# Kernel optimization log

Hardware: AMD Instinct MI355X
Metric: run time of the kernel (lower is better)

## Reference

```python
import jax, jax.numpy as jnp
import numpy as np

N_NODES = 50000
N_EDGES = 600000
N_DISCRETE = 70
NH = N_DISCRETE - 6          # 64
EMB = 128                    # n_embedding
D = NH + EMB                 # 192, resdnn/cross input dim
RES_HID = 512                # l_hidden entries
N_RES = 2                    # len(l_hidden)
N_CROSS = 2
PRED_HID = (2 * NH + 512) // 2  # 320
NEG_SLOPE = 0.01


def setup_inputs() -> dict:
    key = jax.random.key(0)
    ks = jax.random.split(key, 24)
    def w(k, shape, fan_in):
        return (jax.random.normal(k, shape, jnp.float32) / np.sqrt(fan_in)).astype(jnp.float32)
    inp = {
        "discrete_x": jax.random.randint(ks[0], (N_NODES, N_DISCRETE), 0, 100, jnp.int64),
        "edge_index": jax.random.randint(ks[1], (2, N_EDGES), 0, N_NODES, jnp.int64),
        # graph embedding linear + 2 GCN layers
        "w_g0": w(ks[2], (NH, EMB), NH), "b_g0": jnp.zeros((EMB,), jnp.float32),
        "w_gcn1": w(ks[3], (EMB, EMB), EMB), "b_gcn1": jnp.zeros((EMB,), jnp.float32),
        "w_gcn2": w(ks[4], (EMB, EMB), EMB), "b_gcn2": jnp.zeros((EMB,), jnp.float32),
        # ResDNN: N_RES dim-preserving residual bottleneck blocks D->RES_HID->D
        "res_w1": w(ks[5], (N_RES, D, RES_HID), D), "res_b1": jnp.zeros((N_RES, RES_HID), jnp.float32),
        "res_w2": w(ks[6], (N_RES, RES_HID, D), RES_HID), "res_b2": jnp.zeros((N_RES, D), jnp.float32),
        # CrossNet: N_CROSS layers
        "cross_w": w(ks[7], (N_CROSS, D), D), "cross_b": jnp.zeros((N_CROSS, D), jnp.float32),
        # Prediction MLP: 2D -> PRED_HID -> 1, sigmoid
        "p_w1": w(ks[8], (2 * D, PRED_HID), 2 * D), "p_b1": jnp.zeros((PRED_HID,), jnp.float32),
        "p_w2": w(ks[9], (PRED_HID, 1), PRED_HID), "p_b2": jnp.zeros((1,), jnp.float32),
    }
    return inp


def _leaky(x):
    return jax.nn.leaky_relu(x, NEG_SLOPE)


def _gcn_conv(x, W, b, row, col, n):
    # PyG GCNConv: linear, then sym-normalized aggregation over A + I, then bias
    h = x @ W
    deg = jax.ops.segment_sum(jnp.ones(row.shape, x.dtype), col, num_segments=n) + 1.0
    dinv = jax.lax.rsqrt(deg)
    norm = dinv[row] * dinv[col]            # [E]
    msg = h[row] * norm[:, None]            # [E, EMB]  (largest intermediate)
    agg = jax.ops.segment_sum(msg, col, num_segments=n)
    agg = agg + h * (dinv * dinv)[:, None]  # self-loop contribution
    return agg + b


def reference(discrete_x, edge_index, w_g0, b_g0, w_gcn1, b_gcn1, w_gcn2, b_gcn2,
              res_w1, res_b1, res_w2, res_b2, cross_w, cross_b,
              p_w1, p_b1, p_w2, p_b2):
    n = discrete_x.shape[0]
    row, col = edge_index[0], edge_index[1]
    # DiscreteFeatureEmbeddingLayer: map n_discrete_features int cols -> nh float dims
    x_d = discrete_x[:, :NH].astype(jnp.float32)
    # graph branch
    x_g = _leaky(x_d @ w_g0 + b_g0)
    x_g = _leaky(_gcn_conv(x_g, w_gcn1, b_gcn1, row, col, n))
    x_g = _leaky(_gcn_conv(x_g, w_gcn2, b_gcn2, row, col, n))
    x = jnp.concatenate([x_d, x_g], axis=-1)  # [N, D]
    # ResDNN: residual bottleneck blocks
    x_deep = x
    for i in range(N_RES):
        h = _leaky(x_deep @ res_w1[i] + res_b1[i])
        x_deep = _leaky(x_deep + h @ res_w2[i] + res_b2[i])
    # CrossNet (DCN): x_{l+1} = x0 * (x_l . w_l) + b_l + x_l
    x0 = x
    x_cross = x
    for i in range(N_CROSS):
        xw = x_cross @ cross_w[i]            # [N]
        x_cross = x0 * xw[:, None] + cross_b[i] + x_cross
    z = jnp.concatenate([x_deep, x_cross], axis=-1)  # [N, 2D]
    h = _leaky(z @ p_w1 + p_b1)
    y = jax.nn.sigmoid(h @ p_w2 + p_b2)
    return y.squeeze(-1)
```

## Files before the change

kernel.cpp:

```cpp
#include <hip/hip_runtime.h>
#include <math.h>

constexpr int NCOLS   = 70;
constexpr int NH      = 64;
constexpr int EMB     = 128;
constexpr int DD      = 192;
constexpr int RES_HID = 512;
constexpr int PRED_HID= 320;

typedef _Float16 f16x8 __attribute__((ext_vector_type(8)));
typedef float    f32x4 __attribute__((ext_vector_type(4)));
#define MFMA16F(a,b,c) __builtin_amdgcn_mfma_f32_16x16x32_f16((a),(b),(c),0,0,0)

constexpr float LO_SCALE   = 4096.0f;
constexpr float LO_DESCALE = 1.0f/4096.0f;
constexpr float Z_SCALE    = 0.0625f;
constexpr float Z_DESCALE  = 16.0f;

__device__ __forceinline__ float leaky(float x){ return x > 0.f ? x : 0.01f*x; }

__global__ void k_zero(int* p, int n){
  int i = blockIdx.x*256 + threadIdx.x;
  if (i < n) p[i] = 0;
}
__global__ void k_hist(const int* __restrict__ col, int* __restrict__ cnt, int E){
  int e = blockIdx.x*256 + threadIdx.x;
  if (e < E) atomicAdd(&cnt[col[e]], 1);
}
__global__ void k_scanA(const int* __restrict__ cnt, int* __restrict__ bsum, int n){
  __shared__ int s;
  if (threadIdx.x == 0) s = 0;
  __syncthreads();
  int i = blockIdx.x*256 + threadIdx.x;
  int v = (i < n) ? cnt[i] : 0;
  #pragma unroll
  for (int o=32;o;o>>=1) v += __shfl_xor(v, o, 64);
  if ((threadIdx.x & 63) == 0) atomicAdd(&s, v);
  __syncthreads();
  if (threadIdx.x == 0) bsum[blockIdx.x] = s;
}
__global__ void k_scanB(int* bsum, int nb){
  __shared__ int s[256];
  __shared__ int carry;
  if (threadIdx.x == 0) carry = 0;
  __syncthreads();
  for (int start = 0; start < nb; start += 256){
    int i = start + threadIdx.x;
    int v = (i < nb) ? bsum[i] : 0;
    s[threadIdx.x] = v; __syncthreads();
    for (int o=1;o<256;o<<=1){
      int t = (threadIdx.x >= o) ? s[threadIdx.x-o] : 0;
      __syncthreads();
      s[threadIdx.x] += t; __syncthreads();
    }
    if (i < nb) bsum[i] = carry + s[threadIdx.x] - v;
    __syncthreads();
    if (threadIdx.x == 255) carry += s[255];
    __syncthreads();
  }
}
__global__ void k_scanC(const int* __restrict__ cnt, const int* __restrict__ bsum,
                        int* __restrict__ base, int* __restrict__ cursor,
                        float* __restrict__ dinv, int n, int E){
  __shared__ int s[256];
  int i = blockIdx.x*256 + threadIdx.x;
  int v = (i < n) ? cnt[i] : 0;
  s[threadIdx.x] = v; __syncthreads();
  for (int o=1;o<256;o<<=1){
    int t = (threadIdx.x >= o) ? s[threadIdx.x-o] : 0;
    __syncthreads();
    s[threadIdx.x] += t; __syncthreads();
  }
  if (i < n){
    int b = bsum[blockIdx.x] + s[threadIdx.x] - v;
    base[i] = b; cursor[i] = b;
    dinv[i] = rsqrtf((float)(v + 1));
  }
  if (i == n-1) base[n] = E;
}
__global__ void k_fill(const int* __restrict__ row, const int* __restrict__ col,
                       const float* __restrict__ dinv, int* __restrict__ cursor,
                       int2* __restrict__ ebin, int E){
  int e = blockIdx.x*256 + threadIdx.x;
  if (e < E){
    int r = row[e], c = col[e];
    int slot = atomicAdd(&cursor[c], 1);
    ebin[slot] = make_int2(r, __float_as_int(dinv[r]));
  }
}

__global__ void k_wprep_pack(const float* __restrict__ W, _Float16* __restrict__ Wh,
                             _Float16* __restrict__ Wl, int K, int N){
  int idx = blockIdx.x*256 + threadIdx.x;
  if (idx < K*N){
    int k = idx / N, nn = idx - k*N;
    float v = W[idx];
    _Float16 h = (_Float16)v;
    float lo = (v - (float)h)*LO_SCALE;
    int kc = k >> 5, r = k & 31;
    int lane = (nn & 15) | ((r >> 3) << 4);
    int j = r & 7;
    size_t dst = ((size_t)((nn >> 4)*(K >> 5) + kc) << 9) + lane*8 + j;
    Wh[dst] = h;
    Wl[dst] = (_Float16)lo;
  }
}

__global__ void k_embed(const int* __restrict__ dx, float* __restrict__ A, int n){
  int idx = blockIdx.x*256 + threadIdx.x;
  if (idx < n*NH){
    int i = idx >> 6, j = idx & 63;
    A[(size_t)i*DD + j] = (float)dx[(size_t)i*NCOLS + j];
  }
}

template<int K>
__global__ void k_lin(const float* __restrict__ X, int ldx, int xoff,
                      const float* __restrict__ W, const float* __restrict__ bias,
                      float* __restrict__ out, int ldo, int ooff, int n, int act)
{
  constexpr int ST = 20;
  __shared__ __align__(16) float sxT[K*ST];
  int i0 = blockIdx.x*16;
  for (int idx = threadIdx.x; idx < 16*K; idx += 256){
    int t = idx / K, k = idx - t*K;
    int i = i0 + t;
    sxT[k*ST + t] = (i < n) ? X[(size_t)i*ldx + xoff + k] : 0.f;
  }
  __syncthreads();
  int jj = threadIdx.x & 127;
  int tg = threadIdx.x >> 7;
  float b = bias ? bias[jj] : 0.f;
  float acc[8];
  #pragma unroll
  for (int t=0;t<8;t++) acc[t] = b;
  for (int k=0;k<K;k++){
    float w = W[(size_t)k*128 + jj];
    float4 xa = *(const float4*)&sxT[k*ST + tg*8];
    float4 xb = *(const float4*)&sxT[k*ST + tg*8 + 4];
    acc[0] = fmaf(xa.x, w, acc[0]); acc[1] = fmaf(xa.y, w, acc[1]);
    acc[2] = fmaf(xa.z, w, acc[2]); acc[3] = fmaf(xa.w, w, acc[3]);
    acc[4] = fmaf(xb.x, w, acc[4]); acc[5] = fmaf(xb.y, w, acc[5]);
    acc[6] = fmaf(xb.z, w, acc[6]); acc[7] = fmaf(xb.w, w, acc[7]);
  }
  #pragma unroll
  for (int tt=0;tt<8;tt++){
    int i = i0 + tg*8 + tt;
    if (i < n){
      float v = acc[tt];
      if (act) v = leaky(v);
      out[(size_t)i*ldo + ooff + jj] = v;
    }
  }
}

__global__ void k_gather(const float* __restrict__ h, const float* __restrict__ dinv,
                         const int* __restrict__ base, const int2* __restrict__ ebin,
                         const float* __restrict__ bias, float* __restrict__ out,
                         int ldo, int ooff, int n)
{
  int node = blockIdx.x*4 + (threadIdx.x >> 6);
  int lane = threadIdx.x & 63;
  if (node >= n) return;
  int b0 = base[node], b1 = base[node+1];
  float dc = dinv[node];
  float ax = 0.f, ay = 0.f;
  int e = b0;
  for (; e + 1 < b1; e += 2){
    int2 ea = ebin[e], eb = ebin[e+1];
    float2 ha = ((const float2*)(h + (size_t)ea.x*EMB))[lane];
    float2 hb = ((const float2*)(h + (size_t)eb.x*EMB))[lane];
    float da = __int_as_float(ea.y), db = __int_as_float(eb.y);
    ax = fmaf(ha.x, da, ax); ay = fmaf(ha.y, da, ay);
    ax = fmaf(hb.x, db, ax); ay = fmaf(hb.y, db, ay);
  }
  if (e < b1){
    int2 ea = ebin[e];
    float2 ha = ((const float2*)(h + (size_t)ea.x*EMB))[lane];
    float da = __int_as_float(ea.y);
    ax = fmaf(ha.x, da, ax); ay = fmaf(ha.y, da, ay);
  }
  float2 hc = ((const float2*)(h + (size_t)node*EMB))[lane];
  float vx = leaky((ax + hc.x*dc)*dc + bias[2*lane]);
  float vy = leaky((ay + hc.y*dc)*dc + bias[2*lane+1]);
  float* op = out + (size_t)node*ldo + ooff + 2*lane;
  op[0] = vx; op[1] = vy;
}

constexpr int XS = 196;
constexpr int HS = 516;

__global__ __launch_bounds__(256,2)
void k_resblock_mfma(const float* __restrict__ X,
                     const _Float16* __restrict__ W1h, const _Float16* __restrict__ W1l,
                     const float* __restrict__ b1,
                     const _Float16* __restrict__ W2h, const _Float16* __restrict__ W2l,
                     const float* __restrict__ b2,
                     float* __restrict__ out, int n)
{
  __shared__ __align__(16) _Float16 xh[32*XS];
  __shared__ __align__(16) _Float16 xl[32*XS];
  __shared__ __align__(16) _Float16 hh[32*HS];
  int i0 = blockIdx.x*32;
  for (int idx = threadIdx.x; idx < 32*DD; idx += 256){
    int t = idx / DD, k = idx - t*DD;
    int i = i0 + t;
    float v = (i < n) ? X[(size_t)i*DD + k] : 0.f;
    _Float16 h = (_Float16)v;
    xh[t*XS + k] = h;
    xl[t*XS + k] = (_Float16)((v - (float)h)*LO_SCALE);
  }
  __syncthreads();
  int wv = threadIdx.x >> 6, ln = threadIdx.x & 63;
  int cn = ln & 15, kg = ln >> 4;

  {
    f16x8 A0h[6], A0l[6], A1h[6], A1l[6];
    #pragma unroll
    for (int kc=0;kc<6;kc++){
      int k0 = kc*32 + kg*8;
      A0h[kc] = *(const f16x8*)&xh[cn*XS + k0];
      A0l[kc] = *(const f16x8*)&xl[cn*XS + k0];
      A1h[kc] = *(const f16x8*)&xh[(16+cn)*XS + k0];
      A1l[kc] = *(const f16x8*)&xl[(16+cn)*XS + k0];
    }
    float bias1[8];
    #pragma unroll
    for (int ct=0;ct<8;ct++) bias1[ct] = b1[(wv*8+ct)*16 + cn];
    const _Float16* pbh = W1h + ((size_t)(wv*8)*6 << 9) + ln*8;
    const _Float16* pbl = W1l + ((size_t)(wv*8)*6 << 9) + ln*8;
    f16x8 Bh[6], Bl[6];
    #pragma unroll
    for (int kc=0;kc<6;kc++){
      Bh[kc] = *(const f16x8*)(pbh + ((size_t)kc<<9));
      Bl[kc] = *(const f16x8*)(pbl + ((size_t)kc<<9));
    }
    #pragma unroll 1
    for (int ct = 0; ct < 8; ct++){
      f16x8 Bh2[6], Bl2[6];
      if (ct < 7){
        const _Float16* nh = pbh + ((size_t)((ct+1)*6) << 9);
        const _Float16* nl = pbl + ((size_t)((ct+1)*6) << 9);
        #pragma unroll
        for (int kc=0;kc<6;kc++){
          Bh2[kc] = *(const f16x8*)(nh + ((size_t)kc<<9));
          Bl2[kc] = *(const f16x8*)(nl + ((size_t)kc<<9));
        }
      }
      f32x4 acc0={0.f,0.f,0.f,0.f}, accL0={0.f,0.f,0.f,0.f};
      f32x4 acc1={0.f,0.f,0.f,0.f}, accL1={0.f,0.f,0.f,0.f};
      #pragma unroll
      for (int kc=0;kc<6;kc++){
        acc0  = MFMA16F(A0h[kc], Bh[kc], acc0);
        accL0 = MFMA16F(A0l[kc], Bh[kc], accL0);
        accL0 = MFMA16F(A0h[kc], Bl[kc], accL0);
        acc1  = MFMA16F(A1h[kc], Bh[kc], acc1);
        accL1 = MFMA16F(A1l[kc], Bh[kc], accL1);
        accL1 = MFMA16F(A1h[kc], Bl[kc], accL1);
      }
      int n0 = (wv*8+ct)*16;
      float bb = bias1[ct];
      #pragma unroll
      for (int r=0;r<4;r++){
        hh[(kg*4+r)*HS + n0 + cn]    = (_Float16)leaky(acc0[r] + accL0[r]*LO_DESCALE + bb);
        hh[(16+kg*4+r)*HS + n0 + cn] = (_Float16)leaky(acc1[r] + accL1[r]*LO_DESCALE + bb);
      }
      #pragma unroll
      for (int kc=0;kc<6;kc++){ Bh[kc]=Bh2[kc]; Bl[kc]=Bl2[kc]; }
    }
  }
  __syncthreads();

  {
    f32x4 acc[3][2], accL[3][2];
    #pragma unroll
    for (int c=0;c<3;c++){
      #pragma unroll
      for (int g=0;g<2;g++){
        acc[c][g]  = (f32x4){0.f,0.f,0.f,0.f};
        accL[c][g] = (f32x4){0.f,0.f,0.f,0.f};
      }
    }
    f16x8 B2h[3], B2l[3];
    #pragma unroll
    for (int c=0;c<3;c++){
      size_t off = ((size_t)((wv*3+c)*16) << 9) + ln*8;
      B2h[c] = *(const f16x8*)(W2h + off);
      B2l[c] = *(const f16x8*)(W2l + off);
    }
    #pragma unroll 1
    for (int kc=0;kc<16;kc++){
      f16x8 N2h[3], N2l[3];
      if (kc < 15){
        #pragma unroll
        for (int c=0;c<3;c++){
          size_t off = ((size_t)((wv*3+c)*16 + kc + 1) << 9) + ln*8;
          N2h[c] = *(const f16x8*)(W2h + off);
          N2l[c] = *(const f16x8*)(W2l + off);
        }
      }
      int k0 = kc*32 + kg*8;
      f16x8 a0 = *(const f16x8*)&hh[cn*HS + k0];
      f16x8 a1 = *(const f16x8*)&hh[(16+cn)*HS + k0];
      #pragma unroll
      for (int c=0;c<3;c++){
        acc[c][0]  = MFMA16F(a0, B2h[c], acc[c][0]);
        accL[c][0] = MFMA16F(a0, B2l[c], accL[c][0]);
        acc[c][1]  = MFMA16F(a1, B2h[c], acc[c][1]);
        accL[c][1] = MFMA16F(a1, B2l[c], accL[c][1]);
      }
      #pragma unroll
      for (int c=0;c<3;c++){ B2h[c]=N2h[c]; B2l[c]=N2l[c]; }
    }
    #pragma unroll
    for (int c=0;c<3;c++){
      int n0 = (wv*3+c)*16;
      float bb = b2[n0 + cn];
      #pragma unroll
      for (int r=0;r<4;r++){
        int m0 = kg*4 + r, m1 = 16 + kg*4 + r;
        float res0 = (float)xh[m0*XS + n0 + cn] + (float)xl[m0*XS + n0 + cn]*LO_DESCALE;
        float res1 = (float)xh[m1*XS + n0 + cn] + (float)xl[m1*XS + n0 + cn]*LO_DESCALE;
        int ia = i0 + m0, ib = i0 + m1;
        if (ia < n) out[(size_t)ia*DD + n0 + cn] = leaky(res0 + acc[c][0][r] + accL[c][0][r]*LO_DESCALE + bb);
        if (ib < n) out[(size_t)ib*DD + n0 + cn] = leaky(res1 + acc[c][1][r] + accL[c][1][r]*LO_DESCALE + bb);
      }
    }
  }
}

__global__ void k_cross(const float* __restrict__ X0, const float* __restrict__ cw,
                        const float* __restrict__ cb, float* __restrict__ out, int n)
{
  int node = blockIdx.x*4 + (threadIdx.x >> 6);
  int lane = threadIdx.x & 63;
  if (node >= n) return;
  const float* xr = X0 + (size_t)node*DD;
  float v0[3], xc[3];
  #pragma unroll
  for (int m=0;m<3;m++){ v0[m] = xr[lane + 64*m]; xc[m] = v0[m]; }
  #pragma unroll
  for (int l=0;l<2;l++){
    float p = 0.f;
    #pragma unroll
    for (int m=0;m<3;m++) p += xc[m]*cw[l*DD + lane + 64*m];
    #pragma unroll
    for (int off=32; off>0; off>>=1) p += __shfl_xor(p, off, 64);
    #pragma unroll
    for (int m=0;m<3;m++) xc[m] = v0[m]*p + cb[l*DD + lane + 64*m] + xc[m];
  }
  #pragma unroll
  for (int m=0;m<3;m++) out[(size_t)node*DD + lane + 64*m] = xc[m];
}

constexpr int ZS = 392;

__global__ __launch_bounds__(256,3)
void k_pred_mfma(const float* __restrict__ deep, const float* __restrict__ cross,
                 const _Float16* __restrict__ Wh, const _Float16* __restrict__ Wl,
                 const float* __restrict__ b1,
                 const float* __restrict__ w2, const float* __restrict__ b2,
                 float* __restrict__ y, int n)
{
  __shared__ __align__(16) _Float16 zh[32*ZS];
  __shared__ __align__(16) _Float16 zl[32*ZS];
  __shared__ float sred[4][32];
  int i0 = blockIdx.x*32;
  for (int idx = threadIdx.x; idx < 32*2*DD; idx += 256){
    int t = idx / (2*DD), k = idx - t*(2*DD);
    int i = i0 + t;
    float v = 0.f;
    if (i < n) v = (k < DD) ? deep[(size_t)i*DD + k] : cross[(size_t)i*DD + (k - DD)];
    v *= Z_SCALE;
    _Float16 h = (_Float16)v;
    float lo = (v - (float)h)*LO_SCALE;
    zh[t*ZS + k] = h;
    zl[t*ZS + k] = (_Float16)lo;
  }
  __syncthreads();
  int wv = threadIdx.x >> 6, ln = threadIdx.x & 63;
  int cn = ln & 15, kg = ln >> 4;
  float vs0[4] = {0.f,0.f,0.f,0.f};
  float vs1[4] = {0.f,0.f,0.f,0.f};
  #pragma unroll 1
  for (int ct = 0; ct < 5; ct++){
    int nt = wv*5 + ct;
    int n0 = nt*16;
    f32x4 acc0 = {0.f,0.f,0.f,0.f}, accL0 = {0.f,0.f,0.f,0.f};
    f32x4 acc1 = {0.f,0.f,0.f,0.f}, accL1 = {0.f,0.f,0.f,0.f};
    const _Float16* wbh = Wh + ((size_t)nt*12 << 9) + ln*8;
    const _Float16* wbl = Wl + ((size_t)nt*12 << 9) + ln*8;
    #pragma unroll 4
    for (int kc = 0; kc < 12; kc++){
      f16x8 bh = *(const f16x8*)(wbh + (kc << 9));
      f16x8 bl = *(const f16x8*)(wbl + (kc << 9));
      int k0 = kc*32 + kg*8;
      f16x8 a0h = *(const f16x8*)&zh[cn*ZS + k0];
      f16x8 a0l = *(const f16x8*)&zl[cn*ZS + k0];
      f16x8 a1h = *(const f16x8*)&zh[(16+cn)*ZS + k0];
      f16x8 a1l = *(const f16x8*)&zl[(16+cn)*ZS + k0];
      acc0  = MFMA16F(a0h, bh, acc0);
      accL0 = MFMA16F(a0l, bh, accL0);
      accL0 = MFMA16F(a0h, bl, accL0);
      acc1  = MFMA16F(a1h, bh, acc1);
      accL1 = MFMA16F(a1l, bh, accL1);
      accL1 = MFMA16F(a1h, bl, accL1);
    }
    float bb = b1[n0 + cn];
    float ww = w2[n0 + cn];
    #pragma unroll
    for (int r=0;r<4;r++){
      float v0 = (acc0[r] + accL0[r]*LO_DESCALE)*Z_DESCALE + bb;
      float v1 = (acc1[r] + accL1[r]*LO_DESCALE)*Z_DESCALE + bb;
      vs0[r] += leaky(v0)*ww;
      vs1[r] += leaky(v1)*ww;
    }
  }
  #pragma unroll
  for (int r=0;r<4;r++){
    #pragma unroll
    for (int off=1; off<16; off<<=1){
      vs0[r] += __shfl_xor(vs0[r], off, 64);
      vs1[r] += __shfl_xor(vs1[r], off, 64);
    }
  }
  if (cn == 0){
    #pragma unroll
    for (int r=0;r<4;r++){
      sred[wv][kg*4 + r]      = vs0[r];
      sred[wv][16 + kg*4 + r] = vs1[r];
    }
  }
  __syncthreads();
  if (threadIdx.x < 32){
    int m = threadIdx.x;
    float s = sred[0][m] + sred[1][m] + sred[2][m] + sred[3][m] + b2[0];
    int i = i0 + m;
    if (i < n) y[i] = 1.f/(1.f + expf(-s));
  }
}

extern "C" void kernel_launch(void* const* d_in, const int* in_sizes, int n_in,
                              void* d_out, int out_size, void* d_ws, size_t ws_size,
                              hipStream_t stream)
{
  const int*   dx      = (const int*)d_in[0];
  const int*   ei      = (const int*)d_in[1];
  const float* w_g0    = (const float*)d_in[2];
  const float* b_g0    = (const float*)d_in[3];
  const float* w_gcn1  = (const float*)d_in[4];
  const float* b_gcn1  = (const float*)d_in[5];
  const float* w_gcn2  = (const float*)d_in[6];
  const float* b_gcn2  = (const float*)d_in[7];
  const float* res_w1  = (const float*)d_in[8];
  const float* res_b1  = (const float*)d_in[9];
  const float* res_w2  = (const float*)d_in[10];
  const float* res_b2  = (const float*)d_in[11];
  const float* cross_w = (const float*)d_in[12];
  const float* cross_b = (const float*)d_in[13];
  const float* p_w1    = (const float*)d_in[14];
  const float* p_b1    = (const float*)d_in[15];
  const float* p_w2    = (const float*)d_in[16];
  const float* p_b2    = (const float*)d_in[17];
  float* y = (float*)d_out;

  int n = in_sizes[0] / NCOLS;
  int E = in_sizes[1] / 2;
  const int* row = ei;
  const int* col = ei + E;

  float* ws  = (float*)d_ws;
  float* A   = ws;
  float* B   = A  + (size_t)192*n;
  float* G   = B  + (size_t)192*n;
  float* E1  = G;
  float* E2v = G  + (size_t)128*n;
  float* Dx  = G;
  float* dinv= G  + (size_t)256*n;
  int*  cnt    = (int*)(dinv + n);
  int*  base   = cnt + n;
  int*  cursor = base + n + 2;
  int*  bsum   = cursor + n;
  int2* ebin   = (int2*)((((uintptr_t)(bsum + 256)) + 15) & ~(uintptr_t)15);
  _Float16* wt1h = (_Float16*)((((uintptr_t)(ebin + E)) + 15) & ~(uintptr_t)15);
  _Float16* wt1l = wt1h + (size_t)2*RES_HID*DD;
  _Float16* wt2h = wt1l + (size_t)2*RES_HID*DD;
  _Float16* wt2l = wt2h + (size_t)2*RES_HID*DD;
  _Float16* wph  = wt2l + (size_t)2*RES_HID*DD;
  _Float16* wpl  = wph  + (size_t)PRED_HID*2*DD;

  dim3 blk(256);
  int nb = (n + 255)/256;

  {
    int sz = DD*RES_HID;
    k_wprep_pack<<<(sz+255)/256, blk, 0, stream>>>(res_w1,       wt1h,       wt1l,       DD, RES_HID);
    k_wprep_pack<<<(sz+255)/256, blk, 0, stream>>>(res_w1 + sz,  wt1h + sz,  wt1l + sz,  DD, RES_HID);
    k_wprep_pack<<<(sz+255)/256, blk, 0, stream>>>(res_w2,       wt2h,       wt2l,       RES_HID, DD);
    k_wprep_pack<<<(sz+255)/256, blk, 0, stream>>>(res_w2 + sz,  wt2h + sz,  wt2l + sz,  RES_HID, DD);
    int pz = 2*DD*PRED_HID;
    k_wprep_pack<<<(pz+255)/256, blk, 0, stream>>>(p_w1, wph, wpl, 2*DD, PRED_HID);
  }

  k_zero <<<nb, blk, 0, stream>>>(cnt, n);
  k_hist <<<(E+255)/256, blk, 0, stream>>>(col, cnt, E);
  k_scanA<<<nb, blk, 0, stream>>>(cnt, bsum, n);
  k_scanB<<<1, blk, 0, stream>>>(bsum, nb);
  k_scanC<<<nb, blk, 0, stream>>>(cnt, bsum, base, cursor, dinv, n, E);
  k_fill <<<(E+255)/256, blk, 0, stream>>>(row, col, dinv, cursor, ebin, E);

  k_embed<<<(n*NH+255)/256, blk, 0, stream>>>(dx, A, n);
  k_lin<64> <<<(n+15)/16, blk, 0, stream>>>(A, DD, 0, w_g0, b_g0, E1, EMB, 0, n, 1);
  k_lin<128><<<(n+15)/16, blk, 0, stream>>>(E1, EMB, 0, w_gcn1, nullptr, E2v, EMB, 0, n, 0);
  k_gather  <<<(n+3)/4,   blk, 0, stream>>>(E2v, dinv, base, ebin, b_gcn1, E1, EMB, 0, n);
  k_lin<128><<<(n+15)/16, blk, 0, stream>>>(E1, EMB, 0, w_gcn2, nullptr, E2v, EMB, 0, n, 0);
  k_gather  <<<(n+3)/4,   blk, 0, stream>>>(E2v, dinv, base, ebin, b_gcn2, A, DD, NH, n);
  int rbt = (n + 31)/32;
  k_resblock_mfma<<<rbt, blk, 0, stream>>>(A, wt1h, wt1l, res_b1,
                                           wt2h, wt2l, res_b2, B, n);
  k_resblock_mfma<<<rbt, blk, 0, stream>>>(B, wt1h + (size_t)DD*RES_HID, wt1l + (size_t)DD*RES_HID,
                                           res_b1 + RES_HID,
                                           wt2h + (size_t)DD*RES_HID, wt2l + (size_t)DD*RES_HID,
                                           res_b2 + DD, B, n);
  k_cross<<<(n+3)/4, blk, 0, stream>>>(A, cross_w, cross_b, Dx, n);
  k_pred_mfma<<<rbt, blk, 0, stream>>>(B, Dx, wph, wpl, p_b1, p_w2, p_b2, y, n);
}
```

Measured before the change: 684.8 us.

## Move graph linear layers to split-fp16 MFMA and drop resblock LDS input staging

Replaces the scalar FP32 k_lin kernels for the embedding and two GCN linear layers with an MFMA kernel. It uses hi/lo fp16 split weights prepacked by k_wprep_pack. The resblock kernel now loads its input rows straight from global memory into registers instead of staging them in LDS, re-reads the residual from global, and drops the B-fragment prefetch. Occupancy hints rise to 3 blocks per SM. The aim is to put the small GEMMs on matrix cores and free LDS for more occupancy, at the cost of extra weight-prep launches and uncoalesced per-lane global loads.

```diff
diff --git a/kernel.cpp b/kernel.cpp
--- a/kernel.cpp
+++ b/kernel.cpp
@@ -18,6 +18,16 @@
 constexpr float Z_DESCALE  = 16.0f;
 
 __device__ __forceinline__ float leaky(float x){ return x > 0.f ? x : 0.01f*x; }
+
+__device__ __forceinline__ void cvt_hilo(float4 a, float4 b, f16x8& h, f16x8& l){
+  float v[8] = {a.x,a.y,a.z,a.w,b.x,b.y,b.z,b.w};
+  #pragma unroll
+  for (int j=0;j<8;j++){
+    _Float16 hi = (_Float16)v[j];
+    h[j] = hi;
+    l[j] = (_Float16)((v[j] - (float)hi)*LO_SCALE);
+  }
+}
 
 __global__ void k_zero(int* p, int n){
   int i = blockIdx.x*256 + threadIdx.x;
@@ -114,42 +124,57 @@
   }
 }
 
-template<int K>
-__global__ void k_lin(const float* __restrict__ X, int ldx, int xoff,
-                      const float* __restrict__ W, const float* __restrict__ bias,
-                      float* __restrict__ out, int ldo, int ooff, int n, int act)
+template<int KC>
+__global__ __launch_bounds__(256,3)
+void k_lin_mfma(const float* __restrict__ X, int ldx,
+                const _Float16* __restrict__ Wh, const _Float16* __restrict__ Wl,
+                const float* __restrict__ bias,
+                float* __restrict__ out, int ldo, int ooff, int n, int act)
 {
-  constexpr int ST = 20;
-  __shared__ __align__(16) float sxT[K*ST];
-  int i0 = blockIdx.x*16;
-  for (int idx = threadIdx.x; idx < 16*K; idx += 256){
-    int t = idx / K, k = idx - t*K;
-    int i = i0 + t;
-    sxT[k*ST + t] = (i < n) ? X[(size_t)i*ldx + xoff + k] : 0.f;
-  }
-  __syncthreads();
-  int jj = threadIdx.x & 127;
-  int tg = threadIdx.x >> 7;
-  float b = bias ? bias[jj] : 0.f;
-  float acc[8];
-  #pragma unroll
-  for (int t=0;t<8;t++) acc[t] = b;
-  for (int k=0;k<K;k++){
-    float w = W[(size_t)k*128 + jj];
-    float4 xa = *(const float4*)&sxT[k*ST + tg*8];
-    float4 xb = *(const float4*)&sxT[k*ST + tg*8 + 4];
-    acc[0] = fmaf(xa.x, w, acc[0]); acc[1] = fmaf(xa.y, w, acc[1]);
-    acc[2] = fmaf(xa.z, w, acc[2]); acc[3] = fmaf(xa.w, w, acc[3]);
-    acc[4] = fmaf(xb.x, w, acc[4]); acc[5] = fmaf(xb.y, w, acc[5]);
-    acc[6] = fmaf(xb.z, w, acc[6]); acc[7] = fmaf(xb.w, w, acc[7]);
-  }
-  #pragma unroll
-  for (int tt=0;tt<8;tt++){
-    int i = i0 + tg*8 + tt;
-    if (i < n){
-      float v = acc[tt];
-      if (act) v = leaky(v);
-      out[(size_t)i*ldo + ooff + jj] = v;
+  int i0 = blockIdx.x*32;
+  int wv = threadIdx.x >> 6, ln = threadIdx.x & 63;
+  int cn = ln & 15, kg = ln >> 4;
+  bool rr0 = (i0 + cn) < n, rr1 = (i0 + 16 + cn) < n;
+  const float* xr0 = X + (size_t)(i0 + cn)*ldx + kg*8;
+  const float* xr1 = X + (size_t)(i0 + 16 + cn)*ldx + kg*8;
+  float4 zf = {0.f,0.f,0.f,0.f};
+  f16x8 A0h[KC], A0l[KC], A1h[KC], A1l[KC];
+  #pragma unroll
+  for (int kc=0;kc<KC;kc++){
+    float4 a = rr0 ? *(const float4*)(xr0 + kc*32)     : zf;
+    float4 b = rr0 ? *(const float4*)(xr0 + kc*32 + 4) : zf;
+    cvt_hilo(a, b, A0h[kc], A0l[kc]);
+    float4 c = rr1 ? *(const float4*)(xr1 + kc*32)     : zf;
+    float4 d = rr1 ? *(const float4*)(xr1 + kc*32 + 4) : zf;
+    cvt_hilo(c, d, A1h[kc], A1l[kc]);
+  }
+  #pragma unroll
+  for (int t=0;t<2;t++){
+    int nt = wv*2 + t, n0 = nt*16;
+    const _Float16* wbh = Wh + (((size_t)nt*KC) << 9) + ln*8;
+    const _Float16* wbl = Wl + (((size_t)nt*KC) << 9) + ln*8;
+    f32x4 acc0={0.f,0.f,0.f,0.f}, accL0={0.f,0.f,0.f,0.f};
+    f32x4 acc1={0.f,0.f,0.f,0.f}, accL1={0.f,0.f,0.f,0.f};
+    #pragma unroll
+    for (int kc=0;kc<KC;kc++){
+      f16x8 bh = *(const f16x8*)(wbh + ((size_t)kc<<9));
+      f16x8 bl = *(const f16x8*)(wbl + ((size_t)kc<<9));
+      acc0  = MFMA16F(A0h[kc], bh, acc0);
+      accL0 = MFMA16F(A0l[kc], bh, accL0);
+      accL0 = MFMA16F(A0h[kc], bl, accL0);
+      acc1  = MFMA16F(A1h[kc], bh, acc1);
+      accL1 = MFMA16F(A1l[kc], bh, accL1);
+      accL1 = MFMA16F(A1h[kc], bl, accL1);
+    }
+    float bb = bias ? bias[n0 + cn] : 0.f;
+    #pragma unroll
+    for (int r=0;r<4;r++){
+      int ia = i0 + kg*4 + r, ib = ia + 16;
+      float v0 = acc0[r] + accL0[r]*LO_DESCALE + bb;
+      float v1 = acc1[r] + accL1[r]*LO_DESCALE + bb;
+      if (act){ v0 = leaky(v0); v1 = leaky(v1); }
+      if (ia < n) out[(size_t)ia*ldo + ooff + n0 + cn] = v0;
+      if (ib < n) out[(size_t)ib*ldo + ooff + n0 + cn] = v1;
     }
   }
 }
@@ -187,10 +212,9 @@
   op[0] = vx; op[1] = vy;
 }
 
-constexpr int XS = 196;
 constexpr int HS = 516;
 
-__global__ __launch_bounds__(256,2)
+__global__ __launch_bounds__(256,3)
 void k_resblock_mfma(const float* __restrict__ X,
                      const _Float16* __restrict__ W1h, const _Float16* __restrict__ W1l,
                      const float* __restrict__ b1,
@@ -198,79 +222,50 @@
                      const float* __restrict__ b2,
                      float* __restrict__ out, int n)
 {
-  __shared__ __align__(16) _Float16 xh[32*XS];
-  __shared__ __align__(16) _Float16 xl[32*XS];
   __shared__ __align__(16) _Float16 hh[32*HS];
   int i0 = blockIdx.x*32;
-  for (int idx = threadIdx.x; idx < 32*DD; idx += 256){
-    int t = idx / DD, k = idx - t*DD;
-    int i = i0 + t;
-    float v = (i < n) ? X[(size_t)i*DD + k] : 0.f;
-    _Float16 h = (_Float16)v;
-    xh[t*XS + k] = h;
-    xl[t*XS + k] = (_Float16)((v - (float)h)*LO_SCALE);
-  }
-  __syncthreads();
   int wv = threadIdx.x >> 6, ln = threadIdx.x & 63;
   int cn = ln & 15, kg = ln >> 4;
-
-  {
-    f16x8 A0h[6], A0l[6], A1h[6], A1l[6];
+  bool rr0 = (i0 + cn) < n, rr1 = (i0 + 16 + cn) < n;
+  const float* xr0 = X + (size_t)(i0 + cn)*DD + kg*8;
+  const float* xr1 = X + (size_t)(i0 + 16 + cn)*DD + kg*8;
+  float4 zf = {0.f,0.f,0.f,0.f};
+  f16x8 A0h[6], A0l[6], A1h[6], A1l[6];
+  #pragma unroll
+  for (int kc=0;kc<6;kc++){
+    float4 a = rr0 ? *(const float4*)(xr0 + kc*32)     : zf;
+    float4 b = rr0 ? *(const float4*)(xr0 + kc*32 + 4) : zf;
+    cvt_hilo(a, b, A0h[kc], A0l[kc]);
+    float4 c = rr1 ? *(const float4*)(xr1 + kc*32)     : zf;
+    float4 d = rr1 ? *(const float4*)(xr1 + kc*32 + 4) : zf;
+    cvt_hilo(c, d, A1h[kc], A1l[kc]);
+  }
+  #pragma unroll 1
+  for (int ct = 0; ct < 8; ct++){
+    int nt = wv*8 + ct, n0 = nt*16;
+    const _Float16* wbh = W1h + (((size_t)nt*6) << 9) + ln*8;
+    const _Float16* wbl = W1l + (((size_t)nt*6) << 9) + ln*8;
+    f32x4 acc0={0.f,0.f,0.f,0.f}, accL0={0.f,0.f,0.f,0.f};
+    f32x4 acc1={0.f,0.f,0.f,0.f}, accL1={0.f,0.f,0.f,0.f};
     #pragma unroll
     for (int kc=0;kc<6;kc++){
-      int k0 = kc*32 + kg*8;
-      A0h[kc] = *(const f16x8*)&xh[cn*XS + k0];
-      A0l[kc] = *(const f16x8*)&xl[cn*XS + k0];
-      A1h[kc] = *(const f16x8*)&xh[(16+cn)*XS + k0];
-      A1l[kc] = *(const f16x8*)&xl[(16+cn)*XS + k0];
-    }
-    float bias1[8];
-    #pragma unroll
-    for (int ct=0;ct<8;ct++) bias1[ct] = b1[(wv*8+ct)*16 + cn];
-    const _Float16* pbh = W1h + ((size_t)(wv*8)*6 << 9) + ln*8;
-    const _Float16* pbl = W1l + ((size_t)(wv*8)*6 << 9) + ln*8;
-    f16x8 Bh[6], Bl[6];
-    #pragma unroll
-    for (int kc=0;kc<6;kc++){
-      Bh[kc] = *(const f16x8*)(pbh + ((size_t)kc<<9));
-      Bl[kc] = *(const f16x8*)(pbl + ((size_t)kc<<9));
-    }
-    #pragma unroll 1
-    for (int ct = 0; ct < 8; ct++){
-      f16x8 Bh2[6], Bl2[6];
-      if (ct < 7){
-        const _Float16* nh = pbh + ((size_t)((ct+1)*6) << 9);
-        const _Float16* nl = pbl + ((size_t)((ct+1)*6) << 9);
-        #pragma unroll
-        for (int kc=0;kc<6;kc++){
-          Bh2[kc] = *(const f16x8*)(nh + ((size_t)kc<<9));
-          Bl2[kc] = *(const f16x8*)(nl + ((size_t)kc<<9));
-        }
-      }
-      f32x4 acc0={0.f,0.f,0.f,0.f}, accL0={0.f,0.f,0.f,0.f};
-      f32x4 acc1={0.f,0.f,0.f,0.f}, accL1={0.f,0.f,0.f,0.f};
-      #pragma unroll
-      for (int kc=0;kc<6;kc++){
-        acc0  = MFMA16F(A0h[kc], Bh[kc], acc0);
-        accL0 = MFMA16F(A0l[kc], Bh[kc], accL0);
-        accL0 = MFMA16F(A0h[kc], Bl[kc], accL0);
-        acc1  = MFMA16F(A1h[kc], Bh[kc], acc1);
-        accL1 = MFMA16F(A1l[kc], Bh[kc], accL1);
-        accL1 = MFMA16F(A1h[kc], Bl[kc], accL1);
-      }
-      int n0 = (wv*8+ct)*16;
-      float bb = bias1[ct];
-      #pragma unroll
-      for (int r=0;r<4;r++){
-        hh[(kg*4+r)*HS + n0 + cn]    = (_Float16)leaky(acc0[r] + accL0[r]*LO_DESCALE + bb);
-        hh[(16+kg*4+r)*HS + n0 + cn] = (_Float16)leaky(acc1[r] + accL1[r]*LO_DESCALE + bb);
-      }
-      #pragma unroll
-      for (int kc=0;kc<6;kc++){ Bh[kc]=Bh2[kc]; Bl[kc]=Bl2[kc]; }
+      f16x8 bh = *(const f16x8*)(wbh + ((size_t)kc<<9));
+      f16x8 bl = *(const f16x8*)(wbl + ((size_t)kc<<9));
+      acc0  = MFMA16F(A0h[kc], bh, acc0);
+      accL0 = MFMA16F(A0l[kc], bh, accL0);
+      accL0 = MFMA16F(A0h[kc], bl, accL0);
+      acc1  = MFMA16F(A1h[kc], bh, acc1);
+      accL1 = MFMA16F(A1l[kc], bh, accL1);
+      accL1 = MFMA16F(A1h[kc], bl, accL1);
+    }
+    float bb = b1[n0 + cn];
+    #pragma unroll
+    for (int r=0;r<4;r++){
+      hh[(kg*4+r)*HS + n0 + cn]    = (_Float16)leaky(acc0[r] + accL0[r]*LO_DESCALE + bb);
+      hh[(16+kg*4+r)*HS + n0 + cn] = (_Float16)leaky(acc1[r] + accL1[r]*LO_DESCALE + bb);
     }
   }
   __syncthreads();
-
   {
     f32x4 acc[3][2], accL[3][2];
     #pragma unroll
@@ -319,11 +314,15 @@
       #pragma unroll
       for (int r=0;r<4;r++){
         int m0 = kg*4 + r, m1 = 16 + kg*4 + r;
-        float res0 = (float)xh[m0*XS + n0 + cn] + (float)xl[m0*XS + n0 + cn]*LO_DESCALE;
-        float res1 = (float)xh[m1*XS + n0 + cn] + (float)xl[m1*XS + n0 + cn]*LO_DESCALE;
         int ia = i0 + m0, ib = i0 + m1;
-        if (ia < n) out[(size_t)ia*DD + n0 + cn] = leaky(res0 + acc[c][0][r] + accL[c][0][r]*LO_DESCALE + bb);
-        if (ib < n) out[(size_t)ib*DD + n0 + cn] = leaky(res1 + acc[c][1][r] + accL[c][1][r]*LO_DESCALE + bb);
+        if (ia < n){
+          float res = X[(size_t)ia*DD + n0 + cn];
+          out[(size_t)ia*DD + n0 + cn] = leaky(res + acc[c][0][r] + accL[c][0][r]*LO_DESCALE + bb);
+        }
+        if (ib < n){
+          float res = X[(size_t)ib*DD + n0 + cn];
+          out[(size_t)ib*DD + n0 + cn] = leaky(res + acc[c][1][r] + accL[c][1][r]*LO_DESCALE + bb);
+        }
       }
     }
   }
@@ -488,6 +487,12 @@
   _Float16* wt2l = wt2h + (size_t)2*RES_HID*DD;
   _Float16* wph  = wt2l + (size_t)2*RES_HID*DD;
   _Float16* wpl  = wph  + (size_t)PRED_HID*2*DD;
+  _Float16* wg0h = wpl  + (size_t)PRED_HID*2*DD;
+  _Float16* wg0l = wg0h + (size_t)NH*EMB;
+  _Float16* wg1h = wg0l + (size_t)NH*EMB;
+  _Float16* wg1l = wg1h + (size_t)EMB*EMB;
+  _Float16* wg2h = wg1l + (size_t)EMB*EMB;
+  _Float16* wg2l = wg2h + (size_t)EMB*EMB;
 
   dim3 blk(256);
   int nb = (n + 255)/256;
@@ -500,6 +505,9 @@
     k_wprep_pack<<<(sz+255)/256, blk, 0, stream>>>(res_w2 + sz,  wt2h + sz,  wt2l + sz,  RES_HID, DD);
     int pz = 2*DD*PRED_HID;
     k_wprep_pack<<<(pz+255)/256, blk, 0, stream>>>(p_w1, wph, wpl, 2*DD, PRED_HID);
+    k_wprep_pack<<<(NH*EMB+255)/256, blk, 0, stream>>>(w_g0,   wg0h, wg0l, NH,  EMB);
+    k_wprep_pack<<<(EMB*EMB+255)/256, blk, 0, stream>>>(w_gcn1, wg1h, wg1l, EMB, EMB);
+    k_wprep_pack<<<(EMB*EMB+255)/256, blk, 0, stream>>>(w_gcn2, wg2h, wg2l, EMB, EMB);
   }
 
   k_zero <<<nb, blk, 0, stream>>>(cnt, n);
@@ -509,13 +517,13 @@
   k_scanC<<<nb, blk, 0, stream>>>(cnt, bsum, base, cursor, dinv, n, E);
   k_fill <<<(E+255)/256, blk, 0, stream>>>(row, col, dinv, cursor, ebin, E);
 
+  int rbt = (n + 31)/32;
   k_embed<<<(n*NH+255)/256, blk, 0, stream>>>(dx, A, n);
-  k_lin<64> <<<(n+15)/16, blk, 0, stream>>>(A, DD, 0, w_g0, b_g0, E1, EMB, 0, n, 1);
-  k_lin<128><<<(n+15)/16, blk, 0, stream>>>(E1, EMB, 0, w_gcn1, nullptr, E2v, EMB, 0, n, 0);
-  k_gather  <<<(n+3)/4,   blk, 0, stream>>>(E2v, dinv, base, ebin, b_gcn1, E1, EMB, 0, n);
-  k_lin<128><<<(n+15)/16, blk, 0, stream>>>(E1, EMB, 0, w_gcn2, nullptr, E2v, EMB, 0, n, 0);
-  k_gather  <<<(n+3)/4,   blk, 0, stream>>>(E2v, dinv, base, ebin, b_gcn2, A, DD, NH, n);
-  int rbt = (n + 31)/32;
+  k_lin_mfma<2><<<rbt, blk, 0, stream>>>(A, DD, wg0h, wg0l, b_g0, E1, EMB, 0, n, 1);
+  k_lin_mfma<4><<<rbt, blk, 0, stream>>>(E1, EMB, wg1h, wg1l, nullptr, E2v, EMB, 0, n, 0);
+  k_gather  <<<(n+3)/4, blk, 0, stream>>>(E2v, dinv, base, ebin, b_gcn1, E1, EMB, 0, n);
+  k_lin_mfma<4><<<rbt, blk, 0, stream>>>(E1, EMB, wg2h, wg2l, nullptr, E2v, EMB, 0, n, 0);
+  k_gather  <<<(n+3)/4, blk, 0, stream>>>(E2v, dinv, base, ebin, b_gcn2, A, DD, NH, n);
   k_resblock_mfma<<<rbt, blk, 0, stream>>>(A, wt1h, wt1l, res_b1,
                                            wt2h, wt2l, res_b2, B, n);
   k_resblock_mfma<<<rbt, blk, 0, stream>>>(B, wt1h + (size_t)DD*RES_HID, wt1l + (size_t)DD*RES_HID,
```

After: 833.8 us. 21.8% more time.

## Fuse cross network into prediction kernel, merge weight packing, shrink resblock LDS

Applied to the files above, without the earlier changes.

The CrossNet computation moves into the prediction kernel, so each block builds its cross half of z in shared memory instead of writing and re-reading a separate [N,192] buffer. The five weight-packing launches become one kernel (which also packs GCN weights that nothing uses yet), and the zeroing kernel becomes a hipMemsetAsync. The resblock kernel reuses the input tile's shared memory for the hidden buffer and reads the residual from global memory. This lets launch bounds rise to 3 blocks per CU, at the risk of register spills and extra global reads.

```diff
diff --git a/kernel.cpp b/kernel.cpp
--- a/kernel.cpp
+++ b/kernel.cpp
@@ -19,10 +19,6 @@
 
 __device__ __forceinline__ float leaky(float x){ return x > 0.f ? x : 0.01f*x; }
 
-__global__ void k_zero(int* p, int n){
-  int i = blockIdx.x*256 + threadIdx.x;
-  if (i < n) p[i] = 0;
-}
 __global__ void k_hist(const int* __restrict__ col, int* __restrict__ cnt, int E){
   int e = blockIdx.x*256 + threadIdx.x;
   if (e < E) atomicAdd(&cnt[col[e]], 1);
@@ -89,21 +85,40 @@
   }
 }
 
-__global__ void k_wprep_pack(const float* __restrict__ W, _Float16* __restrict__ Wh,
-                             _Float16* __restrict__ Wl, int K, int N){
+__device__ __forceinline__ void pack_one(const float* __restrict__ W,
+                                         _Float16* __restrict__ Wh, _Float16* __restrict__ Wl,
+                                         int K, int N, int local){
+  int k = local / N, nn = local - k*N;
+  float v = W[local];
+  _Float16 h = (_Float16)v;
+  float lo = (v - (float)h)*LO_SCALE;
+  int kc = k >> 5, r = k & 31;
+  int lane = (nn & 15) | ((r >> 3) << 4);
+  int j = r & 7;
+  size_t dst = ((size_t)((nn >> 4)*(K >> 5) + kc) << 9) + lane*8 + j;
+  Wh[dst] = h;
+  Wl[dst] = (_Float16)lo;
+}
+__global__ void k_wprep_all(const float* res_w1, const float* res_w2, const float* p_w1,
+                            const float* w_g0, const float* w_gcn1, const float* w_gcn2,
+                            _Float16* wt1h, _Float16* wt1l, _Float16* wt2h, _Float16* wt2l,
+                            _Float16* wph, _Float16* wpl, _Float16* wg0h, _Float16* wg0l,
+                            _Float16* wg1h, _Float16* wg1l, _Float16* wg2h, _Float16* wg2l)
+{
   int idx = blockIdx.x*256 + threadIdx.x;
-  if (idx < K*N){
-    int k = idx / N, nn = idx - k*N;
-    float v = W[idx];
-    _Float16 h = (_Float16)v;
-    float lo = (v - (float)h)*LO_SCALE;
-    int kc = k >> 5, r = k & 31;
-    int lane = (nn & 15) | ((r >> 3) << 4);
-    int j = r & 7;
-    size_t dst = ((size_t)((nn >> 4)*(K >> 5) + kc) << 9) + lane*8 + j;
-    Wh[dst] = h;
-    Wl[dst] = (_Float16)lo;
-  }
+  constexpr int SZ = DD*RES_HID;
+  constexpr int PZ = 2*DD*PRED_HID;
+  if (idx < SZ)                 pack_one(res_w1,           wt1h,      wt1l,      DD, RES_HID, idx);
+  else if (idx < 2*SZ)          pack_one(res_w1 + SZ,      wt1h + SZ, wt1l + SZ, DD, RES_HID, idx - SZ);
+  else if (idx < 3*SZ)          pack_one(res_w2,           wt2h,      wt2l,      RES_HID, DD, idx - 2*SZ);
+  else if (idx < 4*SZ)          pack_one(res_w2 + SZ,      wt2h + SZ, wt2l + SZ, RES_HID, DD, idx - 3*SZ);
+  else if (idx < 4*SZ + PZ)     pack_one(p_w1,             wph,       wpl,       2*DD, PRED_HID, idx - 4*SZ);
+  else if (idx < 4*SZ + PZ + NH*EMB)
+                                pack_one(w_g0,             wg0h,      wg0l,      NH, EMB, idx - 4*SZ - PZ);
+  else if (idx < 4*SZ + PZ + NH*EMB + EMB*EMB)
+                                pack_one(w_gcn1,           wg1h,      wg1l,      EMB, EMB, idx - 4*SZ - PZ - NH*EMB);
+  else if (idx < 4*SZ + PZ + NH*EMB + 2*EMB*EMB)
+                                pack_one(w_gcn2,           wg2h,      wg2l,      EMB, EMB, idx - 4*SZ - PZ - NH*EMB - EMB*EMB);
 }
 
 __global__ void k_embed(const int* __restrict__ dx, float* __restrict__ A, int n){
@@ -190,7 +205,7 @@
 constexpr int XS = 196;
 constexpr int HS = 516;
 
-__global__ __launch_bounds__(256,2)
+__global__ __launch_bounds__(256,3)
 void k_resblock_mfma(const float* __restrict__ X,
                      const _Float16* __restrict__ W1h, const _Float16* __restrict__ W1l,
                      const float* __restrict__ b1,
@@ -198,9 +213,10 @@
                      const float* __restrict__ b2,
                      float* __restrict__ out, int n)
 {
-  __shared__ __align__(16) _Float16 xh[32*XS];
-  __shared__ __align__(16) _Float16 xl[32*XS];
-  __shared__ __align__(16) _Float16 hh[32*HS];
+  __shared__ __align__(16) _Float16 smem[32*HS];
+  _Float16* xh = smem;
+  _Float16* xl = smem + 32*XS;
+  _Float16* hh = smem;
   int i0 = blockIdx.x*32;
   for (int idx = threadIdx.x; idx < 32*DD; idx += 256){
     int t = idx / DD, k = idx - t*DD;
@@ -213,17 +229,18 @@
   __syncthreads();
   int wv = threadIdx.x >> 6, ln = threadIdx.x & 63;
   int cn = ln & 15, kg = ln >> 4;
+  f16x8 A0h[6], A0l[6], A1h[6], A1l[6];
+  #pragma unroll
+  for (int kc=0;kc<6;kc++){
+    int k0 = kc*32 + kg*8;
+    A0h[kc] = *(const f16x8*)&xh[cn*XS + k0];
+    A0l[kc] = *(const f16x8*)&xl[cn*XS + k0];
+    A1h[kc] = *(const f16x8*)&xh[(16+cn)*XS + k0];
+    A1l[kc] = *(const f16x8*)&xl[(16+cn)*XS + k0];
+  }
+  __syncthreads();
 
   {
-    f16x8 A0h[6], A0l[6], A1h[6], A1l[6];
-    #pragma unroll
-    for (int kc=0;kc<6;kc++){
-      int k0 = kc*32 + kg*8;
-      A0h[kc] = *(const f16x8*)&xh[cn*XS + k0];
-      A0l[kc] = *(const f16x8*)&xl[cn*XS + k0];
-      A1h[kc] = *(const f16x8*)&xh[(16+cn)*XS + k0];
-      A1l[kc] = *(const f16x8*)&xl[(16+cn)*XS + k0];
-    }
     float bias1[8];
     #pragma unroll
     for (int ct=0;ct<8;ct++) bias1[ct] = b1[(wv*8+ct)*16 + cn];
@@ -319,44 +336,25 @@
       #pragma unroll
       for (int r=0;r<4;r++){
         int m0 = kg*4 + r, m1 = 16 + kg*4 + r;
-        float res0 = (float)xh[m0*XS + n0 + cn] + (float)xl[m0*XS + n0 + cn]*LO_DESCALE;
-        float res1 = (float)xh[m1*XS + n0 + cn] + (float)xl[m1*XS + n0 + cn]*LO_DESCALE;
         int ia = i0 + m0, ib = i0 + m1;
-        if (ia < n) out[(size_t)ia*DD + n0 + cn] = leaky(res0 + acc[c][0][r] + accL[c][0][r]*LO_DESCALE + bb);
-        if (ib < n) out[(size_t)ib*DD + n0 + cn] = leaky(res1 + acc[c][1][r] + accL[c][1][r]*LO_DESCALE + bb);
-      }
-    }
-  }
-}
-
-__global__ void k_cross(const float* __restrict__ X0, const float* __restrict__ cw,
-                        const float* __restrict__ cb, float* __restrict__ out, int n)
-{
-  int node = blockIdx.x*4 + (threadIdx.x >> 6);
-  int lane = threadIdx.x & 63;
-  if (node >= n) return;
-  const float* xr = X0 + (size_t)node*DD;
-  float v0[3], xc[3];
-  #pragma unroll
-  for (int m=0;m<3;m++){ v0[m] = xr[lane + 64*m]; xc[m] = v0[m]; }
-  #pragma unroll
-  for (int l=0;l<2;l++){
-    float p = 0.f;
-    #pragma unroll
-    for (int m=0;m<3;m++) p += xc[m]*cw[l*DD + lane + 64*m];
-    #pragma unroll
-    for (int off=32; off>0; off>>=1) p += __shfl_xor(p, off, 64);
-    #pragma unroll
-    for (int m=0;m<3;m++) xc[m] = v0[m]*p + cb[l*DD + lane + 64*m] + xc[m];
-  }
-  #pragma unroll
-  for (int m=0;m<3;m++) out[(size_t)node*DD + lane + 64*m] = xc[m];
+        if (ia < n){
+          float res = X[(size_t)ia*DD + n0 + cn];
+          out[(size_t)ia*DD + n0 + cn] = leaky(res + acc[c][0][r] + accL[c][0][r]*LO_DESCALE + bb);
+        }
+        if (ib < n){
+          float res = X[(size_t)ib*DD + n0 + cn];
+          out[(size_t)ib*DD + n0 + cn] = leaky(res + acc[c][1][r] + accL[c][1][r]*LO_DESCALE + bb);
+        }
+      }
+    }
+  }
 }
 
 constexpr int ZS = 392;
 
 __global__ __launch_bounds__(256,3)
-void k_pred_mfma(const float* __restrict__ deep, const float* __restrict__ cross,
+void k_pred_mfma(const float* __restrict__ deep, const float* __restrict__ X0,
+                 const float* __restrict__ cw, const float* __restrict__ cb,
                  const _Float16* __restrict__ Wh, const _Float16* __restrict__ Wl,
                  const float* __restrict__ b1,
                  const float* __restrict__ w2, const float* __restrict__ b2,
@@ -366,19 +364,47 @@
   __shared__ __align__(16) _Float16 zl[32*ZS];
   __shared__ float sred[4][32];
   int i0 = blockIdx.x*32;
-  for (int idx = threadIdx.x; idx < 32*2*DD; idx += 256){
-    int t = idx / (2*DD), k = idx - t*(2*DD);
+  for (int idx = threadIdx.x; idx < 32*DD; idx += 256){
+    int t = idx / DD, k = idx - t*DD;
     int i = i0 + t;
-    float v = 0.f;
-    if (i < n) v = (k < DD) ? deep[(size_t)i*DD + k] : cross[(size_t)i*DD + (k - DD)];
+    float v = (i < n) ? deep[(size_t)i*DD + k] : 0.f;
     v *= Z_SCALE;
     _Float16 h = (_Float16)v;
-    float lo = (v - (float)h)*LO_SCALE;
     zh[t*ZS + k] = h;
-    zl[t*ZS + k] = (_Float16)lo;
-  }
-  __syncthreads();
+    zl[t*ZS + k] = (_Float16)((v - (float)h)*LO_SCALE);
+  }
   int wv = threadIdx.x >> 6, ln = threadIdx.x & 63;
+  for (int m = 0; m < 8; m++){
+    int t = wv*8 + m;
+    int node = i0 + t;
+    float v0[3], xc[3];
+    if (node < n){
+      const float* xr = X0 + (size_t)node*DD;
+      #pragma unroll
+      for (int q=0;q<3;q++){ v0[q] = xr[ln + 64*q]; xc[q] = v0[q]; }
+      #pragma unroll
+      for (int l=0;l<2;l++){
+        float p = 0.f;
+        #pragma unroll
+        for (int q=0;q<3;q++) p += xc[q]*cw[l*DD + ln + 64*q];
+        #pragma unroll
+        for (int off=32; off>0; off>>=1) p += __shfl_xor(p, off, 64);
+        #pragma unroll
+        for (int q=0;q<3;q++) xc[q] = v0[q]*p + cb[l*DD + ln + 64*q] + xc[q];
+      }
+    } else {
+      #pragma unroll
+      for (int q=0;q<3;q++) xc[q] = 0.f;
+    }
+    #pragma unroll
+    for (int q=0;q<3;q++){
+      float v = xc[q]*Z_SCALE;
+      _Float16 h = (_Float16)v;
+      zh[t*ZS + DD + ln + 64*q] = h;
+      zl[t*ZS + DD + ln + 64*q] = (_Float16)((v - (float)h)*LO_SCALE);
+    }
+  }
+  __syncthreads();
   int cn = ln & 15, kg = ln >> 4;
   float vs0[4] = {0.f,0.f,0.f,0.f};
   float vs1[4] = {0.f,0.f,0.f,0.f};
@@ -475,7 +501,6 @@
   float* G   = B  + (size_t)192*n;
   float* E1  = G;
   float* E2v = G  + (size_t)128*n;
-  float* Dx  = G;
   float* dinv= G  + (size_t)256*n;
   int*  cnt    = (int*)(dinv + n);
   int*  base   = cnt + n;
@@ -488,21 +513,24 @@
   _Float16* wt2l = wt2h + (size_t)2*RES_HID*DD;
   _Float16* wph  = wt2l + (size_t)2*RES_HID*DD;
   _Float16* wpl  = wph  + (size_t)PRED_HID*2*DD;
+  _Float16* wg0h = wpl  + (size_t)PRED_HID*2*DD;
+  _Float16* wg0l = wg0h + (size_t)NH*EMB;
+  _Float16* wg1h = wg0l + (size_t)NH*EMB;
+  _Float16* wg1l = wg1h + (size_t)EMB*EMB;
+  _Float16* wg2h = wg1l + (size_t)EMB*EMB;
+  _Float16* wg2l = wg2h + (size_t)EMB*EMB;
 
   dim3 blk(256);
   int nb = (n + 255)/256;
 
   {
-    int sz = DD*RES_HID;
-    k_wprep_pack<<<(sz+255)/256, blk, 0, stream>>>(res_w1,       wt1h,       wt1l,       DD, RES_HID);
-    k_wprep_pack<<<(sz+255)/256, blk, 0, stream>>>(res_w1 + sz,  wt1h + sz,  wt1l + sz,  DD, RES_HID);
-    k_wprep_pack<<<(sz+255)/256, blk, 0, stream>>>(res_w2,       wt2h,       wt2l,       RES_HID, DD);
-    k_wprep_pack<<<(sz+255)/256, blk, 0, stream>>>(res_w2 + sz,  wt2h + sz,  wt2l + sz,  RES_HID, DD);
-    int pz = 2*DD*PRED_HID;
-    k_wprep_pack<<<(pz+255)/256, blk, 0, stream>>>(p_w1, wph, wpl, 2*DD, PRED_HID);
-  }
-
-  k_zero <<<nb, blk, 0, stream>>>(cnt, n);
+    int total = 4*DD*RES_HID + 2*DD*PRED_HID + NH*EMB + 2*EMB*EMB;
+    k_wprep_all<<<(total+255)/256, blk, 0, stream>>>(res_w1, res_w2, p_w1, w_g0, w_gcn1, w_gcn2,
+                                                     wt1h, wt1l, wt2h, wt2l, wph, wpl,
+                                                     wg0h, wg0l, wg1h, wg1l, wg2h, wg2l);
+  }
+
+  hipMemsetAsync(cnt, 0, (size_t)n*sizeof(int), stream);
   k_hist <<<(E+255)/256, blk, 0, stream>>>(col, cnt, E);
   k_scanA<<<nb, blk, 0, stream>>>(cnt, bsum, n);
   k_scanB<<<1, blk, 0, stream>>>(bsum, nb);
@@ -522,6 +550,5 @@
                                            res_b1 + RES_HID,
                                            wt2h + (size_t)DD*RES_HID, wt2l + (size_t)DD*RES_HID,
                                            res_b2 + DD, B, n);
-  k_cross<<<(n+3)/4, blk, 0, stream>>>(A, cross_w, cross_b, Dx, n);
-  k_pred_mfma<<<rbt, blk, 0, stream>>>(B, Dx, wph, wpl, p_b1, p_w2, p_b2, y, n);
-}
+  k_pred_mfma<<<rbt, blk, 0, stream>>>(B, A, cross_w, cross_b, wph, wpl, p_b1, p_w2, p_b2, y, n);
+}
```

Result: slower. 900.2 us (+31.5%).
